# Kernel optimization log

Measured on AMD Instinct MI355X. Metric: run time of the kernel, lower is better.

The kernel has to match this reference:

```python
import jax, jax.numpy as jnp
import numpy as np

# dims: S slots, B batch, D pred-rep dim, E slot-embedding dim, H hidden/output dim, V per-slot vocab
S, B, D, E, H, V = 7, 4096, 1024, 128, 512, 200
D0 = D + E  # layer-0 LSTM input size


def setup_inputs() -> dict:
    key = jax.random.key(0)
    ks = jax.random.split(key, 12)
    rn = lambda k, shape, s=0.02: jax.random.normal(k, shape, jnp.float32) * s
    return {
        "pred_reps": jax.random.normal(ks[0], (B, D), jnp.float32),
        "slot_labels": jax.random.randint(ks[1], (S, B), 0, V),
        "emb": rn(ks[2], (S, V, E), 1.0),
        # layer 0: per-slot LSTMCell + highway params
        "Wih0": rn(ks[3], (S, 4 * H, D0)), "Whh0": rn(ks[4], (S, 4 * H, H)),
        "bih0": jnp.zeros((S, 4 * H), jnp.float32), "bhh0": jnp.zeros((S, 4 * H), jnp.float32),
        "hwW0": rn(ks[5], (S, H, D0 + H)), "hwb0": jnp.zeros((S, H), jnp.float32),
        "linW0": rn(ks[6], (S, H, D0)),
        # layer 1 (input size = H)
        "Wih1": rn(ks[7], (S, 4 * H, H)), "Whh1": rn(ks[8], (S, 4 * H, H)),
        "bih1": jnp.zeros((S, 4 * H), jnp.float32), "bhh1": jnp.zeros((S, 4 * H), jnp.float32),
        "hwW1": rn(ks[9], (S, H, 2 * H)), "hwb1": jnp.zeros((S, H), jnp.float32),
        "linW1": rn(ks[10], (S, H, H)),
    }


def _lstm_cell(x, h, c, Wih, Whh, bih, bhh):
    # torch LSTMCell: gates ordered i, f, g, o
    gates = x @ Wih.T + bih + h @ Whh.T + bhh
    i, f, g, o = jnp.split(gates, 4, axis=-1)
    c_new = jax.nn.sigmoid(f) * c + jax.nn.sigmoid(i) * jnp.tanh(g)
    h_new = jax.nn.sigmoid(o) * jnp.tanh(c_new)
    return h_new, c_new


def reference(pred_reps, slot_labels, emb, Wih0, Whh0, bih0, bhh0, hwW0, hwb0, linW0,
              Wih1, Whh1, bih1, bhh1, hwW1, hwb1, linW1):
    def step(carry, xs):
        h0, c0, h1, c1 = carry
        (tbl, idx, wih0, whh0, bi0, bh0, hw0, hb0, lw0,
         wih1, whh1, bi1, bh1, hw1, hb1, lw1) = xs
        # per-slot embedding gather + concat with predicate reps  -> [B, D0]
        x = jnp.concatenate([pred_reps, tbl[idx]], axis=-1)
        # layer 0 cell + highway gate
        h0n, c0n = _lstm_cell(x, h0, c0, wih0, whh0, bi0, bh0)
        gate0 = jax.nn.sigmoid(jnp.concatenate([x, h0n], axis=-1) @ hw0.T + hb0)
        x1 = gate0 * h0n + (1.0 - gate0) * (x @ lw0.T)
        # layer 1 cell (its highway output is dead code in the original: curr_input
        # after the last layer is discarded, so we skip it -- same math)
        h1n, c1n = _lstm_cell(x1, h1, c1, wih1, whh1, bi1, bh1)
        return (h0n, c0n, h1n, c1n), None

    init = tuple(jnp.zeros((B, H), pred_reps.dtype) for _ in range(4))
    xs = (emb, slot_labels, Wih0, Whh0, bih0, bhh0, hwW0, hwb0, linW0,
          Wih1, Whh1, bih1, bhh1, hwW1, hwb1, linW1)
    carry, _ = jax.lax.scan(step, init, xs)
    return carry[2]  # last_h: top-layer hidden after final slot
```

## Files before the change

### kernel.cpp

```cpp
#include <hip/hip_runtime.h>
#include <stdint.h>

typedef unsigned short u16;

#define S_   7
#define B_   4096
#define D_   1024
#define E_   128
#define H_   512
#define V_   200
#define D0_  1152
#define KX0  1664
#define KX1  1024
#define G4H  2048

typedef __bf16 bf16x8 __attribute__((ext_vector_type(8)));
typedef float  f32x4  __attribute__((ext_vector_type(4)));
typedef u16    u16x8  __attribute__((ext_vector_type(8)));

__device__ __forceinline__ u16 f2bf(float f) {
  union { float f; uint32_t u; } v; v.f = f;
  uint32_t r = v.u + 0x7fffu + ((v.u >> 16) & 1u);
  return (u16)(r >> 16);
}
__device__ __forceinline__ float bf2f(u16 b) {
  union { uint32_t u; float f; } v; v.u = ((uint32_t)b) << 16;
  return v.f;
}
__device__ __forceinline__ float sigmoidf_(float x) { return 1.0f / (1.0f + __expf(-x)); }
__device__ __forceinline__ float tanhf_(float x) {
  float t = __expf(-2.f * fabsf(x));
  return copysignf((1.f - t) / (1.f + t), x);
}

__device__ __forceinline__ void glds16(const u16* g, u16* l) {
  __builtin_amdgcn_global_load_lds(
      (const __attribute__((address_space(1))) uint32_t*)g,
      (__attribute__((address_space(3))) uint32_t*)l, 16, 0, 0);
}

__device__ __forceinline__ void cvt8(const float* src, u16x8* dst) {
  const float4* p = (const float4*)src;
  float4 x = p[0], y = p[1];
  u16x8 o;
  o[0]=f2bf(x.x); o[1]=f2bf(x.y); o[2]=f2bf(x.z); o[3]=f2bf(x.w);
  o[4]=f2bf(y.x); o[5]=f2bf(y.y); o[6]=f2bf(y.z); o[7]=f2bf(y.w);
  *dst = o;
}

template<int KA, int KB, int KK>
__global__ void pack_gates4(const float* __restrict__ Wih, const float* __restrict__ Whh,
                            u16* __restrict__ dst) {
  const int NG = KK / 8;
  const int stride = gridDim.x * 256;
  int idx = blockIdx.x * 256 + threadIdx.x;
  long daddr[4]; const float* saddr[4];
  #pragma unroll
  for (int u = 0; u < 4; ++u) {
    int i = idx + u * stride;
    int sr = i / NG, kg = i - sr * NG;
    int k8 = kg * 8;
    long s = sr >> 11;
    int  r = sr & 2047;
    int  g = r >> 9, j = r & 511;
    long drow = (s << 11) + ((j >> 4) * 64 + g * 16 + (j & 15));
    daddr[u] = drow * KK + k8;
    saddr[u] = (k8 + 8 <= KA) ? (Wih + (long)sr * KA + k8)
                              : (Whh + (long)sr * KB + (k8 - KA));
  }
  float v[4][8];
  #pragma unroll
  for (int u = 0; u < 4; ++u) {
    const float4* p = (const float4*)saddr[u];
    float4 x = p[0], y = p[1];
    v[u][0]=x.x; v[u][1]=x.y; v[u][2]=x.z; v[u][3]=x.w;
    v[u][4]=y.x; v[u][5]=y.y; v[u][6]=y.z; v[u][7]=y.w;
  }
  #pragma unroll
  for (int u = 0; u < 4; ++u) {
    u16x8 o;
    #pragma unroll
    for (int q = 0; q < 8; ++q) o[q] = f2bf(v[u][q]);
    *(u16x8*)&dst[daddr[u]] = o;
  }
}

template<int KS>
__global__ void pack_hl4(const float* __restrict__ src, u16* __restrict__ dst, int off16) {
  const int NG = KX0 / 8;
  const int stride = gridDim.x * 256;
  int idx = blockIdx.x * 256 + threadIdx.x;
  #pragma unroll
  for (int u = 0; u < 4; ++u) {
    int i = idx + u * stride;
    int sj = i / NG, kg = i - sj * NG;
    int k8 = kg * 8;
    long s = sj >> 9;
    int  j = sj & 511;
    long drow = (s << 10) + ((j >> 4) * 32 + off16 + (j & 15));
    u16x8 o;
    if (k8 + 8 <= KS) {
      cvt8(src + (long)sj * KS + k8, &o);
    } else {
      #pragma unroll
      for (int q = 0; q < 8; ++q) o[q] = 0;
    }
    *(u16x8*)&dst[drow * KX0 + k8] = o;
  }
}

__global__ void pack_pred4(const float* __restrict__ pred, u16* __restrict__ dst) {
  const int NG = KX0 / 8;
  const int stride = gridDim.x * 256;
  int idx = blockIdx.x * 256 + threadIdx.x;
  #pragma unroll
  for (int u = 0; u < 4; ++u) {
    int i = idx + u * stride;
    int row = i / NG, kg = i - row * NG;
    int k8 = kg * 8;
    u16x8 o;
    if (k8 + 8 <= D_) {
      cvt8(pred + (long)row * D_ + k8, &o);
    } else {
      #pragma unroll
      for (int q = 0; q < 8; ++q) o[q] = 0;
    }
    *(u16x8*)&dst[(long)row * KX0 + k8] = o;
  }
}

__global__ void bias_sum(const float* __restrict__ a, const float* __restrict__ b,
                         float* __restrict__ o, int n) {
  int i = blockIdx.x * 256 + threadIdx.x;
  if (i < n) o[i] = a[i] + b[i];
}

__global__ void zero_f(float* __restrict__ p, int n) {
  for (int i = blockIdx.x * 256 + threadIdx.x; i < n; i += gridDim.x * 256) p[i] = 0.f;
}
__global__ void zero_u16k(u16* __restrict__ p, int n) {
  for (int i = blockIdx.x * 256 + threadIdx.x; i < n; i += gridDim.x * 256) p[i] = 0;
}

__global__ void gather_emb(const float* __restrict__ emb_s, const int* __restrict__ idx_s,
                           u16* __restrict__ xcat) {
  long b = blockIdx.x;
  int e = threadIdx.x;
  int ix = idx_s[b];
  xcat[b * KX0 + D_ + e] = f2bf(emb_s[(long)ix * E_ + e]);
}

template<int MODE>
__global__ __launch_bounds__(256)
void gemm_fused(const u16* __restrict__ A, int lda,
                const u16* __restrict__ W, int ldw,
                int K, int ntn, int cpx,
                const float* __restrict__ bsum,
                float* __restrict__ cbuf,
                u16* __restrict__ hdst, int hld, int hoff,
                float* __restrict__ hf32,
                const u16* __restrict__ xcat0) {
  __shared__ __align__(16) u16 lds[(2 + 3) * 8192];
  u16* lA = lds;
  u16* lW = lds + 2 * 8192;
  const int tid  = threadIdx.x;
  const int lane = tid & 63;
  const int wave = tid >> 6;
  const int p    = blockIdx.x;
  const int bid  = (p & 7) * cpx + (p >> 3);
  const int tn = bid % ntn;
  const int tm = bid / ntn;
  const long row0 = (long)tm * 128;
  const long col0 = (long)tn * 128;
  const int wm = (wave >> 1) * 64;
  const int wn = (wave & 1) * 64;
  const int fr = lane & 15;
  const int fk = (lane >> 4) * 8;
  const int wr = wave * 32;

  const int srow = wr + (lane >> 3);
  const int scol = ((lane & 7) ^ ((lane >> 3) & 7)) * 8;
  const u16* ga = A + (row0 + srow) * (long)lda + scol;
  const u16* gw = W + (col0 + srow) * (long)ldw + scol;
  const int dst0 = wr * 64 + lane * 8;

  int aoff[4], woff[4];
  #pragma unroll
  for (int m = 0; m < 4; ++m) aoff[m] = (wm + m * 16 + fr) * 64;
  #pragma unroll
  for (int n = 0; n < 4; ++n) woff[n] = (wn + n * 16 + fr) * 64;
  const int swz = (fr & 7) << 3;
  const int kk0 = (0 + fk) ^ swz;
  const int kk1 = (32 + fk) ^ swz;

  f32x4 acc[4][4] = {};
  const int nt = K >> 6;

  auto stA = [&](int t, int b) {
    const u16* g = ga + ((long)t << 6);
    u16* d = lA + b * 8192 + dst0;
    #pragma unroll
    for (int i = 0; i < 4; ++i) glds16(g + (long)(i * 8) * lda, d + i * 512);
  };
  auto stW = [&](int t, int b) {
    const u16* g = gw + ((long)t << 6);
    u16* d = lW + b * 8192 + dst0;
    #pragma unroll
    for (int i = 0; i < 4; ++i) glds16(g + (long)(i * 8) * ldw, d + i * 512);
  };

  stA(0, 0);
  stW(0, 0);
  stW(1, 1);

  for (int t = 0; t < nt; ++t) {
    if (t + 1 < nt) asm volatile("s_waitcnt vmcnt(4)\n\ts_barrier" ::: "memory");
    else            asm volatile("s_waitcnt vmcnt(0)\n\ts_barrier" ::: "memory");
    if (t + 1 < nt) stA(t + 1, (t + 1) & 1);
    if (t + 2 < nt) stW(t + 2, (t + 2) % 3);

    const u16* Ab = lA + (t & 1) * 8192;
    const u16* Wb = lW + (t % 3) * 8192;
    bf16x8 af0[4], wf0[4], af1[4], wf1[4];
    #pragma unroll
    for (int m = 0; m < 4; ++m) af0[m] = *(const bf16x8*)&Ab[aoff[m] + kk0];
    #pragma unroll
    for (int n = 0; n < 4; ++n) wf0[n] = *(const bf16x8*)&Wb[woff[n] + kk0];
    #pragma unroll
    for (int m = 0; m < 4; ++m) af1[m] = *(const bf16x8*)&Ab[aoff[m] + kk1];
    #pragma unroll
    for (int n = 0; n < 4; ++n) wf1[n] = *(const bf16x8*)&Wb[woff[n] + kk1];
    #pragma unroll
    for (int m = 0; m < 4; ++m)
      #pragma unroll
      for (int n = 0; n < 4; ++n)
        acc[m][n] = __builtin_amdgcn_mfma_f32_16x16x32_bf16(af0[m], wf0[n], acc[m][n], 0, 0, 0);
    #pragma unroll
    for (int m = 0; m < 4; ++m)
      #pragma unroll
      for (int n = 0; n < 4; ++n)
        acc[m][n] = __builtin_amdgcn_mfma_f32_16x16x32_bf16(af1[m], wf1[n], acc[m][n], 0, 0, 0);
  }

  const int cr = (lane >> 4) * 4;
  const int jg = wn >> 6;

  if (MODE == 0) {
    const int j = tn * 32 + jg * 16 + fr;
    const float bi = bsum[j], bf = bsum[512 + j], bg = bsum[1024 + j], bo = bsum[1536 + j];
    #pragma unroll
    for (int m = 0; m < 4; ++m) {
      const long rbase = row0 + wm + m * 16 + cr;
      #pragma unroll
      for (int r = 0; r < 4; ++r) {
        const long ri = rbase + r;
        float gi = acc[m][0][r] + bi;
        float gf = acc[m][1][r] + bf;
        float gg = acc[m][2][r] + bg;
        float go = acc[m][3][r] + bo;
        float cv = cbuf[ri * H_ + j];
        float cn = sigmoidf_(gf) * cv + sigmoidf_(gi) * tanhf_(gg);
        float hn = sigmoidf_(go) * tanhf_(cn);
        cbuf[ri * H_ + j] = cn;
        hdst[ri * hld + hoff + j] = f2bf(hn);
        if (hf32) hf32[ri * H_ + j] = hn;
      }
    }
  } else {
    #pragma unroll
    for (int pp = 0; pp < 2; ++pp) {
      const int j = tn * 64 + jg * 32 + pp * 16 + fr;
      const float bj = bsum[j];
      #pragma unroll
      for (int m = 0; m < 4; ++m) {
        const long rbase = row0 + wm + m * 16 + cr;
        #pragma unroll
        for (int r = 0; r < 4; ++r) {
          const long ri = rbase + r;
          float gv = sigmoidf_(acc[m][2 * pp][r] + bj);
          float h0 = bf2f(xcat0[ri * KX0 + D0_ + j]);
          float x1 = gv * h0 + (1.f - gv) * acc[m][2 * pp + 1][r];
          hdst[ri * hld + hoff + j] = f2bf(x1);
        }
      }
    }
  }
}

extern "C" void kernel_launch(void* const* d_in, const int* in_sizes, int n_in,
                              void* d_out, int out_size, void* d_ws, size_t ws_size,
                              hipStream_t stream) {
  const float* pred   = (const float*)d_in[0];
  const int*   labels = (const int*)d_in[1];
  const float* emb    = (const float*)d_in[2];
  const float* Wih0   = (const float*)d_in[3];
  const float* Whh0   = (const float*)d_in[4];
  const float* bih0   = (const float*)d_in[5];
  const float* bhh0   = (const float*)d_in[6];
  const float* hwW0   = (const float*)d_in[7];
  const float* hwb0   = (const float*)d_in[8];
  const float* linW0  = (const float*)d_in[9];
  const float* Wih1   = (const float*)d_in[10];
  const float* Whh1   = (const float*)d_in[11];
  const float* bih1   = (const float*)d_in[12];
  const float* bhh1   = (const float*)d_in[13];
  float* out = (float*)d_out;

  char* ws = (char*)d_ws;
  size_t off = 0;
  auto alloc = [&](size_t bytes) {
    char* p = ws + off;
    off = (off + bytes + 255) & ~(size_t)255;
    return p;
  };
  u16* WC0   = (u16*)alloc((size_t)S_ * G4H * KX0 * 2);
  u16* WHL   = (u16*)alloc((size_t)S_ * 1024 * KX0 * 2);
  u16* WC1   = (u16*)alloc((size_t)S_ * G4H * KX1 * 2);
  u16* xcat  = (u16*)alloc((size_t)B_ * KX0 * 2);
  u16* x1cat = (u16*)alloc((size_t)B_ * KX1 * 2);
  float* c0   = (float*)alloc((size_t)B_ * H_ * 4);
  float* c1   = (float*)alloc((size_t)B_ * H_ * 4);
  float* bs0  = (float*)alloc((size_t)S_ * G4H * 4);
  float* bs1  = (float*)alloc((size_t)S_ * G4H * 4);

  pack_gates4<D0_, H_, KX0><<<2912, 256, 0, stream>>>(Wih0, Whh0, WC0);
  pack_gates4<H_,  H_, KX1><<<1792, 256, 0, stream>>>(Wih1, Whh1, WC1);
  pack_hl4<KX0><<<728, 256, 0, stream>>>(hwW0,  WHL, 0);
  pack_hl4<D0_><<<728, 256, 0, stream>>>(linW0, WHL, 16);
  pack_pred4<<<832, 256, 0, stream>>>(pred, xcat);
  bias_sum<<<(S_ * G4H + 255) / 256, 256, 0, stream>>>(bih0, bhh0, bs0, S_ * G4H);
  bias_sum<<<(S_ * G4H + 255) / 256, 256, 0, stream>>>(bih1, bhh1, bs1, S_ * G4H);
  zero_f<<<256, 256, 0, stream>>>(c0, B_ * H_);
  zero_f<<<256, 256, 0, stream>>>(c1, B_ * H_);
  zero_u16k<<<256, 256, 0, stream>>>(x1cat, B_ * KX1);

  const int g0 = (B_ / 128) * (G4H / 128);
  const int g1 = (B_ / 128) * (1024 / 128);

  for (int s = 0; s < S_; ++s) {
    gather_emb<<<B_, E_, 0, stream>>>(emb + (size_t)s * V_ * E_, labels + (size_t)s * B_, xcat);

    gemm_fused<0><<<g0, 256, 0, stream>>>(
        xcat, KX0, WC0 + (size_t)s * G4H * KX0, KX0, KX0, G4H / 128, g0 / 8,
        bs0 + (size_t)s * G4H, c0, xcat, KX0, D0_, nullptr, nullptr);

    gemm_fused<1><<<g1, 256, 0, stream>>>(
        xcat, KX0, WHL + (size_t)s * 1024 * KX0, KX0, KX0, 1024 / 128, g1 / 8,
        hwb0 + (size_t)s * H_, nullptr, x1cat, KX1, 0, nullptr, xcat);

    gemm_fused<0><<<g0, 256, 0, stream>>>(
        x1cat, KX1, WC1 + (size_t)s * G4H * KX1, KX1, KX1, G4H / 128, g0 / 8,
        bs1 + (size_t)s * G4H, c1, x1cat, KX1, H_, out, nullptr);
  }
}
```

Measured before the change: 698.2 us.

## Load GEMM A-operand directly into registers and double-buffer only W in LDS

The GEMM kernel stops staging the activation tile A through shared memory. Each wave now loads its A fragments straight from global memory into registers, ping-ponging between two register sets, while W stays in LDS, now double-buffered instead of triple-buffered. The goal is to cut LDS footprint and LDS read traffic, which may allow more resident blocks. The cost is duplicated global A reads across waves sharing the same rows, more register pressure, and a loop that assumes an even number of K tiles.

New measurement: 1.218 ms. 1.74x slower.

```diff
diff --git a/kernel.cpp b/kernel.cpp
--- a/kernel.cpp
+++ b/kernel.cpp
@@ -160,9 +160,7 @@
                 u16* __restrict__ hdst, int hld, int hoff,
                 float* __restrict__ hf32,
                 const u16* __restrict__ xcat0) {
-  __shared__ __align__(16) u16 lds[(2 + 3) * 8192];
-  u16* lA = lds;
-  u16* lW = lds + 2 * 8192;
+  __shared__ __align__(16) u16 lW[2 * 8192];
   const int tid  = threadIdx.x;
   const int lane = tid & 63;
   const int wave = tid >> 6;
@@ -180,13 +178,12 @@
 
   const int srow = wr + (lane >> 3);
   const int scol = ((lane & 7) ^ ((lane >> 3) & 7)) * 8;
-  const u16* ga = A + (row0 + srow) * (long)lda + scol;
   const u16* gw = W + (col0 + srow) * (long)ldw + scol;
   const int dst0 = wr * 64 + lane * 8;
 
-  int aoff[4], woff[4];
-  #pragma unroll
-  for (int m = 0; m < 4; ++m) aoff[m] = (wm + m * 16 + fr) * 64;
+  const u16* Ag = A + (row0 + wm + fr) * (long)lda;
+
+  int woff[4];
   #pragma unroll
   for (int n = 0; n < 4; ++n) woff[n] = (wn + n * 16 + fr) * 64;
   const int swz = (fr & 7) << 3;
@@ -196,50 +193,54 @@
   f32x4 acc[4][4] = {};
   const int nt = K >> 6;
 
-  auto stA = [&](int t, int b) {
-    const u16* g = ga + ((long)t << 6);
-    u16* d = lA + b * 8192 + dst0;
-    #pragma unroll
-    for (int i = 0; i < 4; ++i) glds16(g + (long)(i * 8) * lda, d + i * 512);
-  };
   auto stW = [&](int t, int b) {
     const u16* g = gw + ((long)t << 6);
     u16* d = lW + b * 8192 + dst0;
     #pragma unroll
     for (int i = 0; i < 4; ++i) glds16(g + (long)(i * 8) * ldw, d + i * 512);
   };
-
-  stA(0, 0);
+  auto loadA = [&](int t, bf16x8* a0, bf16x8* a1) {
+    const long k0 = (long)t << 6;
+    #pragma unroll
+    for (int m = 0; m < 4; ++m) {
+      a0[m] = *(const bf16x8*)&Ag[(long)(m * 16) * lda + k0 + fk];
+      a1[m] = *(const bf16x8*)&Ag[(long)(m * 16) * lda + k0 + 32 + fk];
+    }
+  };
+  auto compute = [&](const bf16x8* a0, const bf16x8* a1, const u16* Wb) {
+    bf16x8 wf0[4], wf1[4];
+    #pragma unroll
+    for (int n = 0; n < 4; ++n) wf0[n] = *(const bf16x8*)&Wb[woff[n] + kk0];
+    #pragma unroll
+    for (int n = 0; n < 4; ++n) wf1[n] = *(const bf16x8*)&Wb[woff[n] + kk1];
+    #pragma unroll
+    for (int m = 0; m < 4; ++m)
+      #pragma unroll
+      for (int n = 0; n < 4; ++n)
+        acc[m][n] = __builtin_amdgcn_mfma_f32_16x16x32_bf16(a0[m], wf0[n], acc[m][n], 0, 0, 0);
+    #pragma unroll
+    for (int m = 0; m < 4; ++m)
+      #pragma unroll
+      for (int n = 0; n < 4; ++n)
+        acc[m][n] = __builtin_amdgcn_mfma_f32_16x16x32_bf16(a1[m], wf1[n], acc[m][n], 0, 0, 0);
+  };
+
+  bf16x8 afA0[4], afA1[4], afB0[4], afB1[4];
+
   stW(0, 0);
-  stW(1, 1);
-
-  for (int t = 0; t < nt; ++t) {
-    if (t + 1 < nt) asm volatile("s_waitcnt vmcnt(4)\n\ts_barrier" ::: "memory");
-    else            asm volatile("s_waitcnt vmcnt(0)\n\ts_barrier" ::: "memory");
-    if (t + 1 < nt) stA(t + 1, (t + 1) & 1);
-    if (t + 2 < nt) stW(t + 2, (t + 2) % 3);
-
-    const u16* Ab = lA + (t & 1) * 8192;
-    const u16* Wb = lW + (t % 3) * 8192;
-    bf16x8 af0[4], wf0[4], af1[4], wf1[4];
-    #pragma unroll
-    for (int m = 0; m < 4; ++m) af0[m] = *(const bf16x8*)&Ab[aoff[m] + kk0];
-    #pragma unroll
-    for (int n = 0; n < 4; ++n) wf0[n] = *(const bf16x8*)&Wb[woff[n] + kk0];
-    #pragma unroll
-    for (int m = 0; m < 4; ++m) af1[m] = *(const bf16x8*)&Ab[aoff[m] + kk1];
-    #pragma unroll
-    for (int n = 0; n < 4; ++n) wf1[n] = *(const bf16x8*)&Wb[woff[n] + kk1];
-    #pragma unroll
-    for (int m = 0; m < 4; ++m)
-      #pragma unroll
-      for (int n = 0; n < 4; ++n)
-        acc[m][n] = __builtin_amdgcn_mfma_f32_16x16x32_bf16(af0[m], wf0[n], acc[m][n], 0, 0, 0);
-    #pragma unroll
-    for (int m = 0; m < 4; ++m)
-      #pragma unroll
-      for (int n = 0; n < 4; ++n)
-        acc[m][n] = __builtin_amdgcn_mfma_f32_16x16x32_bf16(af1[m], wf1[n], acc[m][n], 0, 0, 0);
+  loadA(0, afA0, afA1);
+
+  for (int t = 0; t < nt; t += 2) {
+    __syncthreads();
+    stW(t + 1, 1);
+    loadA(t + 1, afB0, afB1);
+    compute(afA0, afA1, lW);
+    __syncthreads();
+    if (t + 2 < nt) {
+      stW(t + 2, 0);
+      loadA(t + 2, afA0, afA1);
+    }
+    compute(afB0, afB1, lW + 8192);
   }
 
   const int cr = (lane >> 4) * 4;
```

## Hoist embedding gather out of slot loop and stream it as separate GEMM K segment

Applied to the files above, without the earlier changes.

Gathers all slot embeddings up front into a dedicated bf16 buffer and has the GEMM read the last K tiles from that buffer, which removes the per-slot gather launch. The activation row becomes [pred | h0 | pad] with a narrower stride, and the weights are re-packed so their K order matches. The GEMM pipeline also changes from a 3-deep W / 2-deep A ring with vmcnt waits to a simple double buffer with __syncthreads, which frees LDS but may expose more load latency.

New measurement: 699.5 us. Within noise of the previous version (+0.2%).

```diff
diff --git a/kernel.cpp b/kernel.cpp
--- a/kernel.cpp
+++ b/kernel.cpp
@@ -10,7 +10,8 @@
 #define H_   512
 #define V_   200
 #define D0_  1152
-#define KX0  1664
+#define XLD  1536
+#define K0_  1664
 #define KX1  1024
 #define G4H  2048
 
@@ -48,84 +49,82 @@
   *dst = o;
 }
 
-template<int KA, int KB, int KK>
-__global__ void pack_gates4(const float* __restrict__ Wih, const float* __restrict__ Whh,
-                            u16* __restrict__ dst) {
-  const int NG = KK / 8;
-  const int stride = gridDim.x * 256;
-  int idx = blockIdx.x * 256 + threadIdx.x;
-  long daddr[4]; const float* saddr[4];
-  #pragma unroll
-  for (int u = 0; u < 4; ++u) {
-    int i = idx + u * stride;
-    int sr = i / NG, kg = i - sr * NG;
-    int k8 = kg * 8;
-    long s = sr >> 11;
-    int  r = sr & 2047;
-    int  g = r >> 9, j = r & 511;
-    long drow = (s << 11) + ((j >> 4) * 64 + g * 16 + (j & 15));
-    daddr[u] = drow * KK + k8;
-    saddr[u] = (k8 + 8 <= KA) ? (Wih + (long)sr * KA + k8)
-                              : (Whh + (long)sr * KB + (k8 - KA));
-  }
-  float v[4][8];
-  #pragma unroll
-  for (int u = 0; u < 4; ++u) {
-    const float4* p = (const float4*)saddr[u];
-    float4 x = p[0], y = p[1];
-    v[u][0]=x.x; v[u][1]=x.y; v[u][2]=x.z; v[u][3]=x.w;
-    v[u][4]=y.x; v[u][5]=y.y; v[u][6]=y.z; v[u][7]=y.w;
-  }
-  #pragma unroll
-  for (int u = 0; u < 4; ++u) {
-    u16x8 o;
-    #pragma unroll
-    for (int q = 0; q < 8; ++q) o[q] = f2bf(v[u][q]);
-    *(u16x8*)&dst[daddr[u]] = o;
-  }
-}
-
-template<int KS>
-__global__ void pack_hl4(const float* __restrict__ src, u16* __restrict__ dst, int off16) {
-  const int NG = KX0 / 8;
-  const int stride = gridDim.x * 256;
-  int idx = blockIdx.x * 256 + threadIdx.x;
-  #pragma unroll
-  for (int u = 0; u < 4; ++u) {
-    int i = idx + u * stride;
-    int sj = i / NG, kg = i - sj * NG;
-    int k8 = kg * 8;
-    long s = sj >> 9;
-    int  j = sj & 511;
-    long drow = (s << 10) + ((j >> 4) * 32 + off16 + (j & 15));
-    u16x8 o;
-    if (k8 + 8 <= KS) {
-      cvt8(src + (long)sj * KS + k8, &o);
-    } else {
-      #pragma unroll
-      for (int q = 0; q < 8; ++q) o[q] = 0;
+template<int KK, int P1, int P2, int KA, int KB>
+__global__ void pack_gw(const float* __restrict__ Wih, const float* __restrict__ Whh,
+                        u16* __restrict__ dst) {
+  const int CH = KK / 32;
+  int i = blockIdx.x * 256 + threadIdx.x;
+  int sr = i / CH, c = i - sr * CH;
+  int k = c * 32;
+  long s = sr >> 11;
+  int  r = sr & 2047;
+  int  g = r >> 9, j = r & 511;
+  long drow = (s << 11) + ((j >> 4) * 64 + g * 16 + (j & 15));
+  const float* src = (k < P1) ? Wih + (long)sr * KA + k
+                   : (k < P2) ? Whh + (long)sr * KB + (k - P1)
+                              : Wih + (long)sr * KA + P1 + (k - P2);
+  u16* d = dst + drow * KK + k;
+  #pragma unroll
+  for (int q = 0; q < 4; ++q) {
+    u16x8 o; cvt8(src + q * 8, &o);
+    *(u16x8*)(d + q * 8) = o;
+  }
+}
+
+template<int KS, bool Z2>
+__global__ void pack_hw(const float* __restrict__ src, u16* __restrict__ dst, int off16) {
+  const int CH = K0_ / 32;
+  int i = blockIdx.x * 256 + threadIdx.x;
+  int sj = i / CH, c = i - sj * CH;
+  int k = c * 32;
+  long s = sj >> 9;
+  int  j = sj & 511;
+  long drow = (s << 10) + ((j >> 4) * 32 + off16 + (j & 15));
+  u16* d = dst + drow * K0_ + k;
+  if (k >= 1024 && k < 1536 && Z2) {
+    u16x8 z = {};
+    #pragma unroll
+    for (int q = 0; q < 4; ++q) *(u16x8*)(d + q * 8) = z;
+    return;
+  }
+  const float* sp = (k < 1024) ? src + (long)sj * KS + k
+                  : (k < 1536) ? src + (long)sj * KS + 1152 + (k - 1024)
+                               : src + (long)sj * KS + 1024 + (k - 1536);
+  #pragma unroll
+  for (int q = 0; q < 4; ++q) {
+    u16x8 o; cvt8(sp + q * 8, &o);
+    *(u16x8*)(d + q * 8) = o;
+  }
+}
+
+__global__ void pack_predz(const float* __restrict__ pred, u16* __restrict__ dst) {
+  const int CH = XLD / 32;
+  int i = blockIdx.x * 256 + threadIdx.x;
+  int row = i / CH, c = i - row * CH;
+  int k = c * 32;
+  u16* d = dst + (long)row * XLD + k;
+  if (k < 1024) {
+    const float* sp = pred + (long)row * D_ + k;
+    #pragma unroll
+    for (int q = 0; q < 4; ++q) {
+      u16x8 o; cvt8(sp + q * 8, &o);
+      *(u16x8*)(d + q * 8) = o;
     }
-    *(u16x8*)&dst[drow * KX0 + k8] = o;
-  }
-}
-
-__global__ void pack_pred4(const float* __restrict__ pred, u16* __restrict__ dst) {
-  const int NG = KX0 / 8;
-  const int stride = gridDim.x * 256;
-  int idx = blockIdx.x * 256 + threadIdx.x;
-  #pragma unroll
-  for (int u = 0; u < 4; ++u) {
-    int i = idx + u * stride;
-    int row = i / NG, kg = i - row * NG;
-    int k8 = kg * 8;
-    u16x8 o;
-    if (k8 + 8 <= D_) {
-      cvt8(pred + (long)row * D_ + k8, &o);
-    } else {
-      #pragma unroll
-      for (int q = 0; q < 8; ++q) o[q] = 0;
-    }
-    *(u16x8*)&dst[(long)row * KX0 + k8] = o;
+  } else {
+    u16x8 z = {};
+    #pragma unroll
+    for (int q = 0; q < 4; ++q) *(u16x8*)(d + q * 8) = z;
+  }
+}
+
+__global__ void xgather(const float* __restrict__ emb, const int* __restrict__ labels,
+                        u16* __restrict__ EMB) {
+  int b = blockIdx.x;
+  int e = threadIdx.x;
+  #pragma unroll
+  for (int s = 0; s < S_; ++s) {
+    int ix = labels[s * B_ + b];
+    EMB[((long)(s * B_ + b)) * E_ + e] = f2bf(emb[((long)(s * V_ + ix)) * E_ + e]);
   }
 }
 
@@ -134,33 +133,25 @@
   int i = blockIdx.x * 256 + threadIdx.x;
   if (i < n) o[i] = a[i] + b[i];
 }
-
 __global__ void zero_f(float* __restrict__ p, int n) {
   for (int i = blockIdx.x * 256 + threadIdx.x; i < n; i += gridDim.x * 256) p[i] = 0.f;
 }
 __global__ void zero_u16k(u16* __restrict__ p, int n) {
   for (int i = blockIdx.x * 256 + threadIdx.x; i < n; i += gridDim.x * 256) p[i] = 0;
-}
-
-__global__ void gather_emb(const float* __restrict__ emb_s, const int* __restrict__ idx_s,
-                           u16* __restrict__ xcat) {
-  long b = blockIdx.x;
-  int e = threadIdx.x;
-  int ix = idx_s[b];
-  xcat[b * KX0 + D_ + e] = f2bf(emb_s[(long)ix * E_ + e]);
 }
 
 template<int MODE>
 __global__ __launch_bounds__(256)
 void gemm_fused(const u16* __restrict__ A, int lda,
+                const u16* __restrict__ EMBs,
                 const u16* __restrict__ W, int ldw,
-                int K, int ntn, int cpx,
+                int K, int TS, int ntn, int cpx,
                 const float* __restrict__ bsum,
                 float* __restrict__ cbuf,
                 u16* __restrict__ hdst, int hld, int hoff,
                 float* __restrict__ hf32,
                 const u16* __restrict__ xcat0) {
-  __shared__ __align__(16) u16 lds[(2 + 3) * 8192];
+  __shared__ __align__(16) u16 lds[4 * 8192];
   u16* lA = lds;
   u16* lW = lds + 2 * 8192;
   const int tid  = threadIdx.x;
@@ -181,8 +172,23 @@
   const int srow = wr + (lane >> 3);
   const int scol = ((lane & 7) ^ ((lane >> 3) & 7)) * 8;
   const u16* ga = A + (row0 + srow) * (long)lda + scol;
+  const u16* ge = EMBs ? (EMBs + (row0 + srow) * (long)E_ + scol) : nullptr;
   const u16* gw = W + (col0 + srow) * (long)ldw + scol;
   const int dst0 = wr * 64 + lane * 8;
+
+  auto stage = [&](int t, int b) {
+    const u16* gb; long ld;
+    if (t < TS) { gb = ga + ((long)t << 6);        ld = lda; }
+    else        { gb = ge + ((long)(t - TS) << 6); ld = E_;  }
+    const u16* gww = gw + ((long)t << 6);
+    u16* dA = lA + b * 8192 + dst0;
+    u16* dW = lW + b * 8192 + dst0;
+    #pragma unroll
+    for (int i = 0; i < 4; ++i) {
+      glds16(gb  + (long)(i * 8) * ld,  dA + i * 512);
+      glds16(gww + (long)(i * 8) * ldw, dW + i * 512);
+    }
+  };
 
   int aoff[4], woff[4];
   #pragma unroll
@@ -196,31 +202,13 @@
   f32x4 acc[4][4] = {};
   const int nt = K >> 6;
 
-  auto stA = [&](int t, int b) {
-    const u16* g = ga + ((long)t << 6);
-    u16* d = lA + b * 8192 + dst0;
-    #pragma unroll
-    for (int i = 0; i < 4; ++i) glds16(g + (long)(i * 8) * lda, d + i * 512);
-  };
-  auto stW = [&](int t, int b) {
-    const u16* g = gw + ((long)t << 6);
-    u16* d = lW + b * 8192 + dst0;
-    #pragma unroll
-    for (int i = 0; i < 4; ++i) glds16(g + (long)(i * 8) * ldw, d + i * 512);
-  };
-
-  stA(0, 0);
-  stW(0, 0);
-  stW(1, 1);
+  stage(0, 0);
 
   for (int t = 0; t < nt; ++t) {
-    if (t + 1 < nt) asm volatile("s_waitcnt vmcnt(4)\n\ts_barrier" ::: "memory");
-    else            asm volatile("s_waitcnt vmcnt(0)\n\ts_barrier" ::: "memory");
-    if (t + 1 < nt) stA(t + 1, (t + 1) & 1);
-    if (t + 2 < nt) stW(t + 2, (t + 2) % 3);
-
+    __syncthreads();
+    if (t + 1 < nt) stage(t + 1, (t + 1) & 1);
     const u16* Ab = lA + (t & 1) * 8192;
-    const u16* Wb = lW + (t % 3) * 8192;
+    const u16* Wb = lW + (t & 1) * 8192;
     bf16x8 af0[4], wf0[4], af1[4], wf1[4];
     #pragma unroll
     for (int m = 0; m < 4; ++m) af0[m] = *(const bf16x8*)&Ab[aoff[m] + kk0];
@@ -278,7 +266,7 @@
         for (int r = 0; r < 4; ++r) {
           const long ri = rbase + r;
           float gv = sigmoidf_(acc[m][2 * pp][r] + bj);
-          float h0 = bf2f(xcat0[ri * KX0 + D0_ + j]);
+          float h0 = bf2f(xcat0[ri * XLD + 1024 + j]);
           float x1 = gv * h0 + (1.f - gv) * acc[m][2 * pp + 1][r];
           hdst[ri * hld + hoff + j] = f2bf(x1);
         }
@@ -313,21 +301,23 @@
     off = (off + bytes + 255) & ~(size_t)255;
     return p;
   };
-  u16* WC0   = (u16*)alloc((size_t)S_ * G4H * KX0 * 2);
-  u16* WHL   = (u16*)alloc((size_t)S_ * 1024 * KX0 * 2);
+  u16* WC0   = (u16*)alloc((size_t)S_ * G4H * K0_ * 2);
+  u16* WHL   = (u16*)alloc((size_t)S_ * 1024 * K0_ * 2);
   u16* WC1   = (u16*)alloc((size_t)S_ * G4H * KX1 * 2);
-  u16* xcat  = (u16*)alloc((size_t)B_ * KX0 * 2);
+  u16* xcat  = (u16*)alloc((size_t)B_ * XLD * 2);
+  u16* EMB   = (u16*)alloc((size_t)S_ * B_ * E_ * 2);
   u16* x1cat = (u16*)alloc((size_t)B_ * KX1 * 2);
   float* c0   = (float*)alloc((size_t)B_ * H_ * 4);
   float* c1   = (float*)alloc((size_t)B_ * H_ * 4);
   float* bs0  = (float*)alloc((size_t)S_ * G4H * 4);
   float* bs1  = (float*)alloc((size_t)S_ * G4H * 4);
 
-  pack_gates4<D0_, H_, KX0><<<2912, 256, 0, stream>>>(Wih0, Whh0, WC0);
-  pack_gates4<H_,  H_, KX1><<<1792, 256, 0, stream>>>(Wih1, Whh1, WC1);
-  pack_hl4<KX0><<<728, 256, 0, stream>>>(hwW0,  WHL, 0);
-  pack_hl4<D0_><<<728, 256, 0, stream>>>(linW0, WHL, 16);
-  pack_pred4<<<832, 256, 0, stream>>>(pred, xcat);
+  pack_gw<K0_, 1024, 1536, D0_, H_><<<2912, 256, 0, stream>>>(Wih0, Whh0, WC0);
+  pack_gw<KX1,  512, 1024, H_,  H_><<<1792, 256, 0, stream>>>(Wih1, Whh1, WC1);
+  pack_hw<K0_, false><<<728, 256, 0, stream>>>(hwW0,  WHL, 0);
+  pack_hw<D0_, true ><<<728, 256, 0, stream>>>(linW0, WHL, 16);
+  pack_predz<<<768, 256, 0, stream>>>(pred, xcat);
+  xgather<<<B_, E_, 0, stream>>>(emb, labels, EMB);
   bias_sum<<<(S_ * G4H + 255) / 256, 256, 0, stream>>>(bih0, bhh0, bs0, S_ * G4H);
   bias_sum<<<(S_ * G4H + 255) / 256, 256, 0, stream>>>(bih1, bhh1, bs1, S_ * G4H);
   zero_f<<<256, 256, 0, stream>>>(c0, B_ * H_);
@@ -338,18 +328,18 @@
   const int g1 = (B_ / 128) * (1024 / 128);
 
   for (int s = 0; s < S_; ++s) {
-    gather_emb<<<B_, E_, 0, stream>>>(emb + (size_t)s * V_ * E_, labels + (size_t)s * B_, xcat);
+    const u16* EMBs = EMB + (size_t)s * B_ * E_;
 
     gemm_fused<0><<<g0, 256, 0, stream>>>(
-        xcat, KX0, WC0 + (size_t)s * G4H * KX0, KX0, KX0, G4H / 128, g0 / 8,
-        bs0 + (size_t)s * G4H, c0, xcat, KX0, D0_, nullptr, nullptr);
+        xcat, XLD, EMBs, WC0 + (size_t)s * G4H * K0_, K0_, K0_, 24, G4H / 128, g0 / 8,
+        bs0 + (size_t)s * G4H, c0, xcat, XLD, 1024, nullptr, nullptr);
 
     gemm_fused<1><<<g1, 256, 0, stream>>>(
-        xcat, KX0, WHL + (size_t)s * 1024 * KX0, KX0, KX0, 1024 / 128, g1 / 8,
+        xcat, XLD, EMBs, WHL + (size_t)s * 1024 * K0_, K0_, K0_, 24, 1024 / 128, g1 / 8,
         hwb0 + (size_t)s * H_, nullptr, x1cat, KX1, 0, nullptr, xcat);
 
     gemm_fused<0><<<g0, 256, 0, stream>>>(
-        x1cat, KX1, WC1 + (size_t)s * G4H * KX1, KX1, KX1, G4H / 128, g0 / 8,
+        x1cat, KX1, nullptr, WC1 + (size_t)s * G4H * KX1, KX1, KX1, 16, G4H / 128, g0 / 8,
         bs1 + (size_t)s * G4H, c1, x1cat, KX1, H_, out, nullptr);
   }
 }
```
